# Optimization experiments

Hardware: AMD Instinct MI355X
Metric: run time of the kernel (lower is better)

## Reference

```python
import jax, jax.numpy as jnp
import numpy as np

GROUPS = 32
EPS = 1e-5


def setup_inputs() -> dict:
    key = jax.random.key(0)
    ks = jax.random.split(key, 4)
    B, C, H, W = 4, 256, 64, 64
    x = jax.random.normal(ks[0], (B, C, H, W), dtype=jnp.float32)
    gn_w = jnp.ones((C,), jnp.float32)
    gn_b = jnp.zeros((C,), jnp.float32)
    qkv_w = jax.random.normal(ks[1], (3 * C, C), dtype=jnp.float32) * (C ** -0.5)
    qkv_b = jnp.zeros((3 * C,), jnp.float32)
    proj_w = jax.random.normal(ks[2], (C, C), dtype=jnp.float32) * (C ** -0.5)
    proj_b = jnp.zeros((C,), jnp.float32)
    return {"x": x, "gn_w": gn_w, "gn_b": gn_b, "qkv_w": qkv_w,
            "qkv_b": qkv_b, "proj_w": proj_w, "proj_b": proj_b}


def _group_norm(x, w, b):
    B, C, H, W = x.shape
    xr = x.reshape(B, GROUPS, -1)                      # [B, G, (C/G)*H*W]
    mean = xr.mean(axis=-1, keepdims=True)
    var = xr.var(axis=-1, keepdims=True)               # biased, like torch
    h = ((xr - mean) * jax.lax.rsqrt(var + EPS)).reshape(B, C, H, W)
    return h * w[None, :, None, None] + b[None, :, None, None]


def reference(x, gn_w, gn_b, qkv_w, qkv_b, proj_w, proj_b):
    B, C, H, W = x.shape
    h = _group_norm(x, gn_w, gn_b)
    # 1x1 conv == channel GEMM
    qkv = jnp.einsum('oc,bchw->bohw', qkv_w, h) + qkv_b[None, :, None, None]
    qkv = qkv.reshape(B, 3, C, H * W)
    q, k, v = qkv[:, 0], qkv[:, 1], qkv[:, 2]          # [B, C, N]
    scale = C ** (-0.5)
    attn = jax.nn.softmax(jnp.einsum('bci,bcj->bij', q, k) * scale, axis=-1)
    out = jnp.einsum('bij,bcj->bci', attn, v).reshape(B, C, H, W)
    out = jnp.einsum('oc,bchw->bohw', proj_w, out) + proj_b[None, :, None, None]
    return x + out
```

## Files before the change

### kernel.cpp

```cpp
#include <hip/hip_runtime.h>
#include <hip/hip_bf16.h>
#include <math.h>

typedef __bf16 bf16;
typedef __bf16 bf16x8 __attribute__((ext_vector_type(8)));
typedef __bf16 bf16x4 __attribute__((ext_vector_type(4)));
typedef float f32x4 __attribute__((ext_vector_type(4)));
typedef float f32x16 __attribute__((ext_vector_type(16)));

#define MFMA16(a, b, c) __builtin_amdgcn_mfma_f32_16x16x32_bf16(a, b, c, 0, 0, 0)
#define MFMA32(a, b, c) __builtin_amdgcn_mfma_f32_32x32x16_bf16(a, b, c, 0, 0, 0)

#define SCALEK 0.09016844005555896f

typedef const __attribute__((address_space(1))) void* gas_t;
typedef __attribute__((address_space(3))) void* las_t;

__global__ __launch_bounds__(256) void gn_stats(const float* __restrict__ x,
                                                float* __restrict__ pstats,
                                                const float* __restrict__ qw,
                                                bf16* __restrict__ qwb) {
  const int bid = blockIdx.x;
  const float* xp = x + (size_t)bid * 4096;
  const int tid = threadIdx.x;

  if (bid < 192) {
    int t = bid * 256 + tid;
    float4 v = *(const float4*)(qw + (size_t)t * 4);
    bf16x4 o;
    o[0] = (bf16)v.x; o[1] = (bf16)v.y; o[2] = (bf16)v.z; o[3] = (bf16)v.w;
    *(bf16x4*)(qwb + (size_t)t * 4) = o;
  }

  float s = 0.f, ss = 0.f;
#pragma unroll
  for (int i = 0; i < 4; ++i) {
    float4 v = *(const float4*)(xp + tid * 4 + i * 1024);
    s += v.x + v.y + v.z + v.w;
    ss += v.x * v.x + v.y * v.y + v.z * v.z + v.w * v.w;
  }
#pragma unroll
  for (int off = 32; off; off >>= 1) {
    s += __shfl_down(s, off);
    ss += __shfl_down(ss, off);
  }
  __shared__ float red[8];
  if ((tid & 63) == 0) {
    red[(tid >> 6) * 2] = s;
    red[(tid >> 6) * 2 + 1] = ss;
  }
  __syncthreads();
  if (tid == 0) {
    pstats[bid * 2] = red[0] + red[2] + red[4] + red[6];
    pstats[bid * 2 + 1] = red[1] + red[3] + red[5] + red[7];
  }
}

__global__ __launch_bounds__(256) void gn_apply(
    const float* __restrict__ x, const float* __restrict__ pstats,
    const float* __restrict__ gw, const float* __restrict__ gb,
    bf16* __restrict__ h) {
  const int bid = blockIdx.x;
  const int c = bid & 255;
  const int gbase = bid & ~7;
  const float* xp = x + (size_t)bid * 4096;
  bf16* hp = h + (size_t)bid * 4096;
  const int tid = threadIdx.x;

  float s = 0.f, ss = 0.f;
#pragma unroll
  for (int i = 0; i < 8; ++i) {
    s += pstats[(gbase + i) * 2];
    ss += pstats[(gbase + i) * 2 + 1];
  }
  const float mean = s * (1.f / 32768.f);
  const float var = ss * (1.f / 32768.f) - mean * mean;
  const float rstd = rsqrtf(var + 1e-5f);
  const float a = gw[c] * rstd;
  const float b2 = gb[c] - mean * a;

#pragma unroll
  for (int i = 0; i < 4; ++i) {
    float4 v = *(const float4*)(xp + tid * 4 + i * 1024);
    bf16x4 o;
    o[0] = (bf16)(v.x * a + b2);
    o[1] = (bf16)(v.y * a + b2);
    o[2] = (bf16)(v.z * a + b2);
    o[3] = (bf16)(v.w * a + b2);
    *(bf16x4*)(hp + tid * 4 + i * 1024) = o;
  }
}

__global__ __launch_bounds__(256) void qkv_gemm(
    const bf16* __restrict__ h, const bf16* __restrict__ wb,
    const float* __restrict__ bias, bf16* __restrict__ qt,
    bf16* __restrict__ kt, bf16* __restrict__ vcm) {
  const int b = blockIdx.z;
  const int o0 = blockIdx.y * 64;
  const int p0 = blockIdx.x * 64;
  __shared__ bf16 Alds[2][64][32];
  __shared__ bf16 Blds[2][64][56];
  const int tid = threadIdx.x;
  const int lane = tid & 63, wid = tid >> 6;
  const int lr = lane & 15, lg = lane >> 4;
  const int wm = wid >> 1, wn = wid & 1;
  const bf16* hb = h + (size_t)b * 256 * 4096;

  const int arow = tid >> 2, ac8 = (tid & 3) * 8;
  const int bcc = tid >> 3, bp8 = (tid & 7) * 8;

#define QKV_STAGE_A(K0, BUF)                                                  \
  __builtin_amdgcn_global_load_lds(                                           \
      (gas_t)(const void*)(wb + (size_t)(o0 + arow) * 256 + (K0) + ac8),      \
      (las_t)(void*)(&Alds[BUF][0][0] + tid * 8), 16, 0, 0);

  f32x4 acc[2][2] = {};

  QKV_STAGE_A(0, 0);
  {
    bf16x8 v = *(const bf16x8*)(hb + (size_t)bcc * 4096 + p0 + bp8);
#pragma unroll
    for (int e = 0; e < 8; ++e) Blds[0][bp8 + e][bcc] = v[e];
  }
  __syncthreads();

  for (int k = 0; k < 8; ++k) {
    const int cur = k & 1, nb = cur ^ 1;
    if (k < 7) {
      QKV_STAGE_A((k + 1) * 32, nb);
      bf16x8 v =
          *(const bf16x8*)(hb + (size_t)((k + 1) * 32 + bcc) * 4096 + p0 + bp8);
#pragma unroll
      for (int e = 0; e < 8; ++e) Blds[nb][bp8 + e][bcc] = v[e];
    }
    bf16x8 af[2], bfr[2];
#pragma unroll
    for (int mi = 0; mi < 2; ++mi)
      af[mi] = *(const bf16x8*)&Alds[cur][wm * 32 + mi * 16 + lr][lg * 8];
#pragma unroll
    for (int ni = 0; ni < 2; ++ni)
      bfr[ni] = *(const bf16x8*)&Blds[cur][wn * 32 + ni * 16 + lr][lg * 8];
#pragma unroll
    for (int mi = 0; mi < 2; ++mi)
#pragma unroll
      for (int ni = 0; ni < 2; ++ni)
        acc[mi][ni] = MFMA16(af[mi], bfr[ni], acc[mi][ni]);
    __syncthreads();
  }
#undef QKV_STAGE_A

#pragma unroll
  for (int mi = 0; mi < 2; ++mi) {
#pragma unroll
    for (int ni = 0; ni < 2; ++ni) {
#pragma unroll
      for (int r = 0; r < 4; ++r) {
        int o = o0 + wm * 32 + mi * 16 + lg * 4 + r;
        int p = p0 + wn * 32 + ni * 16 + lr;
        float val = acc[mi][ni][r] + bias[o];
        if (o < 256) {
          qt[((size_t)b * 4096 + p) * 256 + o] = (bf16)val;
        } else if (o < 512) {
          kt[((size_t)b * 4096 + p) * 256 + (o - 256)] = (bf16)(val * SCALEK);
        } else {
          vcm[((size_t)b * 256 + (o - 512)) * 4096 + p] = (bf16)val;
        }
      }
    }
  }
}

template <int S>
__global__ __launch_bounds__(512, 2) void flash_attn(
    const bf16* __restrict__ qt, const bf16* __restrict__ kt,
    const bf16* __restrict__ vcm, bf16* __restrict__ Opart,
    float* __restrict__ l_g) {
  constexpr int NCOMBO = 4 * S;
  constexpr int CSH = (S == 4) ? 4 : (S == 2) ? 3 : 2;
  constexpr int NIT = (4096 / S) / 32;
  const int bid = blockIdx.x;
  const int combo = bid & (NCOMBO - 1);
  const int qtile = bid >> CSH;
  const int b = combo & 3;
  const int split = combo >> 2;
  const int i0 = qtile * 256;
  const int jbase = split * (4096 / S);

  __shared__ bf16 Klds[2][32][256];
  __shared__ bf16 Vlds[2][256][32];
  const int tid = threadIdx.x;
  const int lane = tid & 63, w = tid >> 6;
  const int ln = lane & 31;
  const int hv = lane >> 5;
  const bf16* qb = qt + (size_t)b * 4096 * 256;
  const bf16* kb = kt + (size_t)b * 4096 * 256;
  const bf16* vb = vcm + (size_t)b * 256 * 4096;

  const int qrow = i0 + w * 32 + ln;
  bf16x8 qf[16];
#pragma unroll
  for (int ks = 0; ks < 16; ++ks)
    qf[ks] = *(const bf16x8*)(qb + (size_t)qrow * 256 + ks * 16 + hv * 8);

  int koff[2], voff[2];
#pragma unroll
  for (int it = 0; it < 2; ++it) {
    int chunk = tid + 512 * it;
    int krow = chunk >> 5;
    koff[it] = krow * 256 + ((((chunk & 31) ^ (krow & 7)) * 8));
    int vrow = chunk >> 2;
    voff[it] = vrow * 4096 + (((chunk & 3) ^ ((vrow >> 2) & 3)) * 8);
  }

#define STAGE_K(JT, BUF)                                                      \
  {                                                                           \
    const int j0s = jbase + (JT) * 32;                                        \
    _Pragma("unroll") for (int it = 0; it < 2; ++it) {                        \
      int chunk = tid + 512 * it;                                             \
      __builtin_amdgcn_global_load_lds(                                       \
          (gas_t)(const void*)(kb + (size_t)j0s * 256 + koff[it]),            \
          (las_t)(void*)(&Klds[BUF][0][0] + chunk * 8), 16, 0, 0);            \
    }                                                                         \
  }
#define STAGE_V(JT, BUF)                                                      \
  {                                                                           \
    const int j0s = jbase + (JT) * 32;                                        \
    _Pragma("unroll") for (int it = 0; it < 2; ++it) {                        \
      int chunk = tid + 512 * it;                                             \
      __builtin_amdgcn_global_load_lds(                                       \
          (gas_t)(const void*)(vb + (size_t)j0s + voff[it]),                  \
          (las_t)(void*)(&Vlds[BUF][0][0] + chunk * 8), 16, 0, 0);            \
    }                                                                         \
  }

  float llane = 0.f;
  f32x16 accO[8] = {};
  const int kswz = ln & 7;
  const int vswz = (ln >> 2) & 3;

  STAGE_K(0, 0);
  STAGE_V(0, 0);
  asm volatile("s_waitcnt vmcnt(0)" ::: "memory");
  __builtin_amdgcn_s_barrier();

  f32x16 a0 = {}, a1 = {};
#pragma unroll
  for (int ks = 0; ks < 8; ++ks) {
    bf16x8 kf0 = *(const bf16x8*)&Klds[0][ln][((2 * ks + hv) ^ kswz) * 8];
    bf16x8 kf1 =
        *(const bf16x8*)&Klds[0][ln][((2 * (ks + 8) + hv) ^ kswz) * 8];
    a0 = MFMA32(kf0, qf[ks], a0);
    a1 = MFMA32(kf1, qf[ks + 8], a1);
  }
  if (NIT > 1) STAGE_K(1, 1);

  for (int t = 0; t < NIT; ++t) {
    asm volatile("s_waitcnt vmcnt(0)" ::: "memory");
    __builtin_amdgcn_s_barrier();

    if (t + 1 < NIT) STAGE_V(t + 1, (t + 1) & 1);
    if (t + 2 < NIT) STAGE_K(t + 2, t & 1);

    float pv[16];
#pragma unroll
    for (int r = 0; r < 16; ++r) pv[r] = exp2f(a0[r] + a1[r]);
    llane += (((pv[0] + pv[1]) + (pv[2] + pv[3])) +
              ((pv[4] + pv[5]) + (pv[6] + pv[7]))) +
             (((pv[8] + pv[9]) + (pv[10] + pv[11])) +
              ((pv[12] + pv[13]) + (pv[14] + pv[15])));

    int pk[8];
#pragma unroll
    for (int q4 = 0; q4 < 8; ++q4)
      asm("v_cvt_pk_bf16_f32 %0, %1, %2"
          : "=v"(pk[q4])
          : "v"(pv[q4 * 2]), "v"(pv[q4 * 2 + 1]));
    bf16x8 pfrag[2];
#pragma unroll
    for (int s = 0; s < 2; ++s) {
      int xa = pk[s * 4 + 0], ya = pk[s * 4 + 2];
      int xb = pk[s * 4 + 1], yb = pk[s * 4 + 3];
      asm("v_permlane32_swap_b32 %0, %1" : "+v"(xa), "+v"(ya));
      asm("v_permlane32_swap_b32 %0, %1" : "+v"(xb), "+v"(yb));
      union { int i[4]; bf16x8 v; } u;
      u.i[0] = xa; u.i[1] = xb; u.i[2] = ya; u.i[3] = yb;
      pfrag[s] = u.v;
    }

    const bf16(*Kc)[256] = Klds[(t + 1) & 1];
    const bf16(*Vc)[32] = Vlds[t & 1];
    __builtin_amdgcn_s_setprio(1);
    if (t + 1 < NIT) {
      f32x16 n0 = {}, n1 = {};
#pragma unroll
      for (int u = 0; u < 8; ++u) {
        bf16x8 kf0 = *(const bf16x8*)&Kc[ln][((2 * u + hv) ^ kswz) * 8];
        n0 = MFMA32(kf0, qf[u], n0);
        bf16x8 kf1 =
            *(const bf16x8*)&Kc[ln][((2 * (u + 8) + hv) ^ kswz) * 8];
        n1 = MFMA32(kf1, qf[u + 8], n1);
        bf16x8 vf0 = *(const bf16x8*)&Vc[u * 32 + ln][((hv) ^ vswz) * 8];
        accO[u] = MFMA32(vf0, pfrag[0], accO[u]);
        bf16x8 vf1 = *(const bf16x8*)&Vc[u * 32 + ln][((2 + hv) ^ vswz) * 8];
        accO[u] = MFMA32(vf1, pfrag[1], accO[u]);
      }
      a0 = n0;
      a1 = n1;
    } else {
#pragma unroll
      for (int u = 0; u < 8; ++u) {
        bf16x8 vf0 = *(const bf16x8*)&Vc[u * 32 + ln][((hv) ^ vswz) * 8];
        accO[u] = MFMA32(vf0, pfrag[0], accO[u]);
        bf16x8 vf1 = *(const bf16x8*)&Vc[u * 32 + ln][((2 + hv) ^ vswz) * 8];
        accO[u] = MFMA32(vf1, pfrag[1], accO[u]);
      }
    }
    __builtin_amdgcn_s_setprio(0);
  }
#undef STAGE_K
#undef STAGE_V

  bf16* ob = Opart + ((size_t)(split * 4 + b) * 4096 + qrow) * 256;
#pragma unroll
  for (int cb = 0; cb < 8; ++cb) {
#pragma unroll
    for (int g = 0; g < 4; ++g) {
      int lo, hi;
      asm("v_cvt_pk_bf16_f32 %0, %1, %2"
          : "=v"(lo)
          : "v"(accO[cb][g * 4 + 0]), "v"(accO[cb][g * 4 + 1]));
      asm("v_cvt_pk_bf16_f32 %0, %1, %2"
          : "=v"(hi)
          : "v"(accO[cb][g * 4 + 2]), "v"(accO[cb][g * 4 + 3]));
      int2 val; val.x = lo; val.y = hi;
      *(int2*)(ob + cb * 32 + g * 8 + hv * 4) = val;
    }
  }
  {
    int xa = __float_as_int(llane);
    int ya = xa;
    asm("v_permlane32_swap_b32 %0, %1" : "+v"(xa), "+v"(ya));
    float ltot = __int_as_float(xa) + __int_as_float(ya);
    if (hv == 0)
      l_g[(size_t)(split * 4 + b) * 4096 + qrow] = ltot;
  }
}

template <int S>
__global__ __launch_bounds__(256) void proj_fused(
    const bf16* __restrict__ Opart, const float* __restrict__ l_g,
    const float* __restrict__ w, const float* __restrict__ bias,
    const float* __restrict__ x, float* __restrict__ out) {
  const int b = blockIdx.y;
  const int p0 = blockIdx.x * 64;
  __shared__ bf16 Wlds[256][32];
  __shared__ bf16 Blds[64][32];
  __shared__ float Linv[64];
  const int tid = threadIdx.x;
  const int lane = tid & 63, wid = tid >> 6;
  const int lr = lane & 15, lg = lane >> 4;

  if (tid < 64) {
    float L = 0.f;
#pragma unroll
    for (int s = 0; s < S; ++s)
      L += l_g[(size_t)(s * 4 + b) * 4096 + p0 + tid];
    Linv[tid] = 1.f / L;
  }
  __syncthreads();

  const int pr = tid >> 2, c8b = (tid & 3) * 8;
  const float invp = Linv[pr];

  float4 wreg[4][2];
  bf16x8 breg[S];

#define PROJ_READ(K0)                                                         \
  {                                                                           \
    _Pragma("unroll") for (int it = 0; it < 4; ++it) {                        \
      int chunk = tid + 256 * it;                                             \
      int row = chunk >> 2, c8 = (chunk & 3) * 8;                             \
      const float* src = w + (size_t)row * 256 + (K0) + c8;                   \
      wreg[it][0] = *(const float4*)src;                                      \
      wreg[it][1] = *(const float4*)(src + 4);                                \
    }                                                                         \
    _Pragma("unroll") for (int s = 0; s < S; ++s) breg[s] =                   \
        *(const bf16x8*)(Opart +                                              \
                         ((size_t)(s * 4 + b) * 4096 + p0 + pr) * 256 +       \
                         (K0) + c8b);                                         \
  }
#define PROJ_WRITE()                                                          \
  {                                                                           \
    _Pragma("unroll") for (int it = 0; it < 4; ++it) {                        \
      int chunk = tid + 256 * it;                                             \
      int row = chunk >> 2, c8 = (chunk & 3) * 8;                             \
      bf16x8 bv;                                                              \
      bv[0] = (bf16)wreg[it][0].x; bv[1] = (bf16)wreg[it][0].y;               \
      bv[2] = (bf16)wreg[it][0].z; bv[3] = (bf16)wreg[it][0].w;               \
      bv[4] = (bf16)wreg[it][1].x; bv[5] = (bf16)wreg[it][1].y;               \
      bv[6] = (bf16)wreg[it][1].z; bv[7] = (bf16)wreg[it][1].w;               \
      *(bf16x8*)&Wlds[row][c8] = bv;                                          \
    }                                                                         \
    {                                                                         \
      float a8[8] = {};                                                       \
      _Pragma("unroll") for (int s = 0; s < S; ++s) {                         \
        _Pragma("unroll") for (int e = 0; e < 8; ++e) a8[e] +=                \
            (float)breg[s][e];                                                \
      }                                                                       \
      bf16x8 bv;                                                              \
      _Pragma("unroll") for (int e = 0; e < 8; ++e) bv[e] =                   \
          (bf16)(a8[e] * invp);                                               \
      *(bf16x8*)&Blds[pr][c8b] = bv;                                          \
    }                                                                         \
  }

  f32x4 acc[4][4] = {};

  PROJ_READ(0);
  PROJ_WRITE();
  __syncthreads();

  for (int k = 0; k < 8; ++k) {
    if (k < 7) PROJ_READ((k + 1) * 32);

    bf16x8 af[4], bfr[4];
#pragma unroll
    for (int mi = 0; mi < 4; ++mi)
      af[mi] = *(const bf16x8*)&Wlds[wid * 64 + mi * 16 + lr][lg * 8];
#pragma unroll
    for (int ni = 0; ni < 4; ++ni)
      bfr[ni] = *(const bf16x8*)&Blds[ni * 16 + lr][lg * 8];
#pragma unroll
    for (int mi = 0; mi < 4; ++mi)
#pragma unroll
      for (int ni = 0; ni < 4; ++ni)
        acc[mi][ni] = MFMA16(af[mi], bfr[ni], acc[mi][ni]);

    __syncthreads();
    if (k < 7) {
      PROJ_WRITE();
      __syncthreads();
    }
  }
#undef PROJ_READ
#undef PROJ_WRITE

#pragma unroll
  for (int mi = 0; mi < 4; ++mi) {
#pragma unroll
    for (int ni = 0; ni < 4; ++ni) {
#pragma unroll
      for (int r = 0; r < 4; ++r) {
        int o = wid * 64 + mi * 16 + lg * 4 + r;
        int p = p0 + ni * 16 + lr;
        size_t idx = ((size_t)b * 256 + o) * 4096 + p;
        out[idx] = acc[mi][ni][r] + bias[o] + x[idx];
      }
    }
  }
}

extern "C" void kernel_launch(void* const* d_in, const int* in_sizes, int n_in,
                              void* d_out, int out_size, void* d_ws,
                              size_t ws_size, hipStream_t stream) {
  (void)in_sizes; (void)n_in; (void)out_size;
  const float* x = (const float*)d_in[0];
  const float* gn_w = (const float*)d_in[1];
  const float* gn_b = (const float*)d_in[2];
  const float* qkv_w = (const float*)d_in[3];
  const float* qkv_b = (const float*)d_in[4];
  const float* proj_w = (const float*)d_in[5];
  const float* proj_b = (const float*)d_in[6];
  float* out = (float*)d_out;

  const size_t MB = 1024ull * 1024ull;
  char* ws = (char*)d_ws;
  bf16* h = (bf16*)(ws);
  bf16* qt = (bf16*)(ws + 8 * MB);
  bf16* kt = (bf16*)(ws + 16 * MB);
  bf16* vcm = (bf16*)(ws + 24 * MB);

  int S;
  if (ws_size >= 32 * MB + 4 * 8 * MB + 4ull * 16384 * sizeof(float) + 8192)
    S = 4;
  else if (ws_size >= 32 * MB + 2 * 8 * MB + 2ull * 16384 * sizeof(float) + 8192)
    S = 2;
  else
    S = 1;

  bf16* Opart;
  float* l_g;
  bf16* qwb;
  if (S >= 2) {
    Opart = (bf16*)(ws + 32 * MB);
    l_g = (float*)(ws + 32 * MB + (size_t)S * 8 * MB);
    qwb = Opart;
  } else {
    Opart = h;
    l_g = (float*)(ws + 32 * MB);
    qwb = (bf16*)(ws + 32 * MB + 512 * 1024);
  }
  float* pstats = l_g + (size_t)S * 16384;

  gn_stats<<<1024, 256, 0, stream>>>(x, pstats, qkv_w, qwb);
  gn_apply<<<1024, 256, 0, stream>>>(x, pstats, gn_w, gn_b, h);
  qkv_gemm<<<dim3(64, 12, 4), 256, 0, stream>>>(h, qwb, qkv_b, qt, kt, vcm);
  if (S == 4) {
    flash_attn<4><<<16 * 16, 512, 0, stream>>>(qt, kt, vcm, Opart, l_g);
    proj_fused<4><<<dim3(64, 4), 256, 0, stream>>>(Opart, l_g, proj_w, proj_b,
                                                   x, out);
  } else if (S == 2) {
    flash_attn<2><<<16 * 8, 512, 0, stream>>>(qt, kt, vcm, Opart, l_g);
    proj_fused<2><<<dim3(64, 4), 256, 0, stream>>>(Opart, l_g, proj_w, proj_b,
                                                   x, out);
  } else {
    flash_attn<1><<<16 * 4, 512, 0, stream>>>(qt, kt, vcm, Opart, l_g);
    proj_fused<1><<<dim3(64, 4), 256, 0, stream>>>(Opart, l_g, proj_w, proj_b,
                                                   x, out);
  }
}
```

Baseline: 154.6 us.

## Double flash-attention KV tile to 64 keys per iteration with one block per CU

Each iteration of the flash attention loop now processes 64 keys instead of 32. The K and V LDS buffers double, with a new V swizzle for 64-wide rows, and the QK, softmax-pack and PV steps each run twice per iteration. The aim is to halve the number of barriers and waitcnt syncs and give more MFMA work between them. The cost is more LDS and registers, so launch bounds drop to one block per CU, which lowers occupancy and latency hiding.

```diff
diff --git a/kernel.cpp b/kernel.cpp
--- a/kernel.cpp
+++ b/kernel.cpp
@@ -171,13 +171,13 @@
 }
 
 template <int S>
-__global__ __launch_bounds__(512, 2) void flash_attn(
+__global__ __launch_bounds__(512, 1) void flash_attn(
     const bf16* __restrict__ qt, const bf16* __restrict__ kt,
     const bf16* __restrict__ vcm, bf16* __restrict__ Opart,
     float* __restrict__ l_g) {
   constexpr int NCOMBO = 4 * S;
   constexpr int CSH = (S == 4) ? 4 : (S == 2) ? 3 : 2;
-  constexpr int NIT = (4096 / S) / 32;
+  constexpr int NIT = (4096 / S) / 64;
   const int bid = blockIdx.x;
   const int combo = bid & (NCOMBO - 1);
   const int qtile = bid >> CSH;
@@ -186,8 +186,8 @@
   const int i0 = qtile * 256;
   const int jbase = split * (4096 / S);
 
-  __shared__ bf16 Klds[2][32][256];
-  __shared__ bf16 Vlds[2][256][32];
+  __shared__ bf16 Klds[2][64][256];
+  __shared__ bf16 Vlds[2][256][64];
   const int tid = threadIdx.x;
   const int lane = tid & 63, w = tid >> 6;
   const int ln = lane & 31;
@@ -202,20 +202,20 @@
   for (int ks = 0; ks < 16; ++ks)
     qf[ks] = *(const bf16x8*)(qb + (size_t)qrow * 256 + ks * 16 + hv * 8);
 
-  int koff[2], voff[2];
-#pragma unroll
-  for (int it = 0; it < 2; ++it) {
+  int koff[4], voff[4];
+#pragma unroll
+  for (int it = 0; it < 4; ++it) {
     int chunk = tid + 512 * it;
     int krow = chunk >> 5;
-    koff[it] = krow * 256 + ((((chunk & 31) ^ (krow & 7)) * 8));
-    int vrow = chunk >> 2;
-    voff[it] = vrow * 4096 + (((chunk & 3) ^ ((vrow >> 2) & 3)) * 8);
+    koff[it] = krow * 256 + (((chunk & 31) ^ (krow & 7)) * 8);
+    int vrow = chunk >> 3;
+    voff[it] = vrow * 4096 + (((chunk & 7) ^ (vrow & 7)) * 8);
   }
 
 #define STAGE_K(JT, BUF)                                                      \
   {                                                                           \
-    const int j0s = jbase + (JT) * 32;                                        \
-    _Pragma("unroll") for (int it = 0; it < 2; ++it) {                        \
+    const int j0s = jbase + (JT) * 64;                                        \
+    _Pragma("unroll") for (int it = 0; it < 4; ++it) {                        \
       int chunk = tid + 512 * it;                                             \
       __builtin_amdgcn_global_load_lds(                                       \
           (gas_t)(const void*)(kb + (size_t)j0s * 256 + koff[it]),            \
@@ -224,8 +224,8 @@
   }
 #define STAGE_V(JT, BUF)                                                      \
   {                                                                           \
-    const int j0s = jbase + (JT) * 32;                                        \
-    _Pragma("unroll") for (int it = 0; it < 2; ++it) {                        \
+    const int j0s = jbase + (JT) * 64;                                        \
+    _Pragma("unroll") for (int it = 0; it < 4; ++it) {                        \
       int chunk = tid + 512 * it;                                             \
       __builtin_amdgcn_global_load_lds(                                       \
           (gas_t)(const void*)(vb + (size_t)j0s + voff[it]),                  \
@@ -233,25 +233,67 @@
     }                                                                         \
   }
 
+#define QK_TILE(KC, A00, A10, A01, A11)                                       \
+  {                                                                           \
+    _Pragma("unroll") for (int ks = 0; ks < 8; ++ks) {                        \
+      bf16x8 kf0 = *(const bf16x8*)&(KC)[ln][((2 * ks + hv) ^ kswz) * 8];     \
+      bf16x8 kf1 =                                                            \
+          *(const bf16x8*)&(KC)[ln][((2 * (ks + 8) + hv) ^ kswz) * 8];        \
+      (A00) = MFMA32(kf0, qf[ks], (A00));                                     \
+      (A10) = MFMA32(kf1, qf[ks + 8], (A10));                                 \
+      bf16x8 kg0 =                                                            \
+          *(const bf16x8*)&(KC)[32 + ln][((2 * ks + hv) ^ kswz) * 8];         \
+      bf16x8 kg1 =                                                            \
+          *(const bf16x8*)&(KC)[32 + ln][((2 * (ks + 8) + hv) ^ kswz) * 8];   \
+      (A01) = MFMA32(kg0, qf[ks], (A01));                                     \
+      (A11) = MFMA32(kg1, qf[ks + 8], (A11));                                 \
+    }                                                                         \
+  }
+
+#define SOFTPACK(A0, A1, PF0, PF1)                                            \
+  {                                                                           \
+    float pv[16];                                                             \
+    _Pragma("unroll") for (int r = 0; r < 16; ++r) pv[r] =                    \
+        exp2f((A0)[r] + (A1)[r]);                                             \
+    llane += (((pv[0] + pv[1]) + (pv[2] + pv[3])) +                           \
+              ((pv[4] + pv[5]) + (pv[6] + pv[7]))) +                          \
+             (((pv[8] + pv[9]) + (pv[10] + pv[11])) +                         \
+              ((pv[12] + pv[13]) + (pv[14] + pv[15])));                       \
+    int pk[8];                                                                \
+    _Pragma("unroll") for (int q4 = 0; q4 < 8; ++q4)                          \
+        asm("v_cvt_pk_bf16_f32 %0, %1, %2"                                    \
+            : "=v"(pk[q4])                                                    \
+            : "v"(pv[q4 * 2]), "v"(pv[q4 * 2 + 1]));                          \
+    {                                                                         \
+      int xa = pk[0], ya = pk[2], xb = pk[1], yb = pk[3];                     \
+      asm("v_permlane32_swap_b32 %0, %1" : "+v"(xa), "+v"(ya));               \
+      asm("v_permlane32_swap_b32 %0, %1" : "+v"(xb), "+v"(yb));               \
+      union { int i[4]; bf16x8 v; } u;                                        \
+      u.i[0] = xa; u.i[1] = xb; u.i[2] = ya; u.i[3] = yb;                     \
+      (PF0) = u.v;                                                            \
+    }                                                                         \
+    {                                                                         \
+      int xa = pk[4], ya = pk[6], xb = pk[5], yb = pk[7];                     \
+      asm("v_permlane32_swap_b32 %0, %1" : "+v"(xa), "+v"(ya));               \
+      asm("v_permlane32_swap_b32 %0, %1" : "+v"(xb), "+v"(yb));               \
+      union { int i[4]; bf16x8 v; } u;                                        \
+      u.i[0] = xa; u.i[1] = xb; u.i[2] = ya; u.i[3] = yb;                     \
+      (PF1) = u.v;                                                            \
+    }                                                                         \
+  }
+
   float llane = 0.f;
   f32x16 accO[8] = {};
   const int kswz = ln & 7;
-  const int vswz = (ln >> 2) & 3;
+  const int vswz = ln & 7;
 
   STAGE_K(0, 0);
   STAGE_V(0, 0);
   asm volatile("s_waitcnt vmcnt(0)" ::: "memory");
   __builtin_amdgcn_s_barrier();
 
-  f32x16 a0 = {}, a1 = {};
-#pragma unroll
-  for (int ks = 0; ks < 8; ++ks) {
-    bf16x8 kf0 = *(const bf16x8*)&Klds[0][ln][((2 * ks + hv) ^ kswz) * 8];
-    bf16x8 kf1 =
-        *(const bf16x8*)&Klds[0][ln][((2 * (ks + 8) + hv) ^ kswz) * 8];
-    a0 = MFMA32(kf0, qf[ks], a0);
-    a1 = MFMA32(kf1, qf[ks + 8], a1);
-  }
+  f32x16 a00 = {}, a10 = {}, a01 = {}, a11 = {};
+  QK_TILE(Klds[0], a00, a10, a01, a11);
   if (NIT > 1) STAGE_K(1, 1);
 
   for (int t = 0; t < NIT; ++t) {
@@ -261,51 +303,37 @@
     if (t + 1 < NIT) STAGE_V(t + 1, (t + 1) & 1);
     if (t + 2 < NIT) STAGE_K(t + 2, t & 1);
 
-    float pv[16];
-#pragma unroll
-    for (int r = 0; r < 16; ++r) pv[r] = exp2f(a0[r] + a1[r]);
-    llane += (((pv[0] + pv[1]) + (pv[2] + pv[3])) +
-              ((pv[4] + pv[5]) + (pv[6] + pv[7]))) +
-             (((pv[8] + pv[9]) + (pv[10] + pv[11])) +
-              ((pv[12] + pv[13]) + (pv[14] + pv[15])));
-
-    int pk[8];
-#pragma unroll
-    for (int q4 = 0; q4 < 8; ++q4)
-      asm("v_cvt_pk_bf16_f32 %0, %1, %2"
-          : "=v"(pk[q4])
-          : "v"(pv[q4 * 2]), "v"(pv[q4 * 2 + 1]));
-    bf16x8 pfrag[2];
-#pragma unroll
-    for (int s = 0; s < 2; ++s) {
-      int xa = pk[s * 4 + 0], ya = pk[s * 4 + 2];
-      int xb = pk[s * 4 + 1], yb = pk[s * 4 + 3];
-      asm("v_permlane32_swap_b32 %0, %1" : "+v"(xa), "+v"(ya));
-      asm("v_permlane32_swap_b32 %0, %1" : "+v"(xb), "+v"(yb));
-      union { int i[4]; bf16x8 v; } u;
-      u.i[0] = xa; u.i[1] = xb; u.i[2] = ya; u.i[3] = yb;
-      pfrag[s] = u.v;
-    }
+    bf16x8 pfrag[4];
+    SOFTPACK(a00, a10, pfrag[0], pfrag[1]);
+    SOFTPACK(a01, a11, pfrag[2], pfrag[3]);
 
     const bf16(*Kc)[256] = Klds[(t + 1) & 1];
-    const bf16(*Vc)[32] = Vlds[t & 1];
+    const bf16(*Vc)[64] = Vlds[t & 1];
     __builtin_amdgcn_s_setprio(1);
     if (t + 1 < NIT) {
-      f32x16 n0 = {}, n1 = {};
+      f32x16 n00 = {}, n10 = {}, n01 = {}, n11 = {};
 #pragma unroll
       for (int u = 0; u < 8; ++u) {
         bf16x8 kf0 = *(const bf16x8*)&Kc[ln][((2 * u + hv) ^ kswz) * 8];
-        n0 = MFMA32(kf0, qf[u], n0);
+        n00 = MFMA32(kf0, qf[u], n00);
         bf16x8 kf1 =
             *(const bf16x8*)&Kc[ln][((2 * (u + 8) + hv) ^ kswz) * 8];
-        n1 = MFMA32(kf1, qf[u + 8], n1);
+        n10 = MFMA32(kf1, qf[u + 8], n10);
+        bf16x8 kg0 = *(const bf16x8*)&Kc[32 + ln][((2 * u + hv) ^ kswz) * 8];
+        n01 = MFMA32(kg0, qf[u], n01);
+        bf16x8 kg1 =
+            *(const bf16x8*)&Kc[32 + ln][((2 * (u + 8) + hv) ^ kswz) * 8];
+        n11 = MFMA32(kg1, qf[u + 8], n11);
         bf16x8 vf0 = *(const bf16x8*)&Vc[u * 32 + ln][((hv) ^ vswz) * 8];
         accO[u] = MFMA32(vf0, pfrag[0], accO[u]);
         bf16x8 vf1 = *(const bf16x8*)&Vc[u * 32 + ln][((2 + hv) ^ vswz) * 8];
         accO[u] = MFMA32(vf1, pfrag[1], accO[u]);
+        bf16x8 vf2 = *(const bf16x8*)&Vc[u * 32 + ln][((4 + hv) ^ vswz) * 8];
+        accO[u] = MFMA32(vf2, pfrag[2], accO[u]);
+        bf16x8 vf3 = *(const bf16x8*)&Vc[u * 32 + ln][((6 + hv) ^ vswz) * 8];
+        accO[u] = MFMA32(vf3, pfrag[3], accO[u]);
       }
-      a0 = n0;
-      a1 = n1;
+      a00 = n00; a10 = n10; a01 = n01; a11 = n11;
     } else {
 #pragma unroll
       for (int u = 0; u < 8; ++u) {
@@ -313,12 +341,18 @@
         accO[u] = MFMA32(vf0, pfrag[0], accO[u]);
         bf16x8 vf1 = *(const bf16x8*)&Vc[u * 32 + ln][((2 + hv) ^ vswz) * 8];
         accO[u] = MFMA32(vf1, pfrag[1], accO[u]);
+        bf16x8 vf2 = *(const bf16x8*)&Vc[u * 32 + ln][((4 + hv) ^ vswz) * 8];
+        accO[u] = MFMA32(vf2, pfrag[2], accO[u]);
+        bf16x8 vf3 = *(const bf16x8*)&Vc[u * 32 + ln][((6 + hv) ^ vswz) * 8];
+        accO[u] = MFMA32(vf3, pfrag[3], accO[u]);
       }
     }
     __builtin_amdgcn_s_setprio(0);
   }
 #undef STAGE_K
 #undef STAGE_V
+#undef QK_TILE
+#undef SOFTPACK
 
   bf16* ob = Opart + ((size_t)(split * 4 + b) * 4096 + qrow) * 256;
 #pragma unroll
```

New measurement: 224.4 us. 45.1% more time.
